# Kernel optimization log

Hardware: AMD Instinct MI355X
Metric: run time of the kernel (lower is better)

Reference implementation:

```python
import jax, jax.numpy as jnp
import numpy as np

NEG_FILL = jnp.finfo(jnp.float32).min  # stands in for tf.float64.min (overflows to -inf in f32)


def setup_inputs() -> dict:
    key = jax.random.key(0)
    k0, k1, k2, k3, k4 = jax.random.split(key, 5)
    B, N, E, D = 4, 4096, 1024, 256
    STD = 0.05  # tf.random_normal_initializer default stddev
    inputs = jax.random.normal(k0, (B, N, E), dtype=jnp.float32)
    Wq = STD * jax.random.normal(k1, (E, D), dtype=jnp.float32)
    Wk = STD * jax.random.normal(k2, (E, D), dtype=jnp.float32)
    Wvdown = STD * jax.random.normal(k3, (E, D), dtype=jnp.float32)
    Wvup = STD * jax.random.normal(k4, (D, E), dtype=jnp.float32)
    return {"inputs": inputs, "Wq": Wq, "Wk": Wk, "Wvdown": Wvdown, "Wvup": Wvup}


def reference(inputs, Wq, Wk, Wvdown, Wvup):
    B, N, E = inputs.shape
    D = Wq.shape[1]
    Q = inputs @ Wq                                   # [B, N, D]
    K = inputs @ Wk                                   # [B, N, D]
    score = jnp.einsum("bqd,bkd->bqk", Q, K)          # [B, N, N]
    score = score / jnp.sqrt(jnp.float32(D))
    # tf.linalg.band_part(score, -1, 0): keep lower triangle (causal)
    causal = jnp.tril(jnp.ones((N, N), dtype=bool))
    score = jnp.where(causal, score, 0.0)
    # original quirk: any exactly-zero entry (including masked ones) -> huge negative
    score = jnp.where(score != 0, score, NEG_FILL)
    attn = jax.nn.softmax(score, axis=-1)             # [B, N, N]
    V = inputs @ (Wvdown @ Wvup)                      # low-rank value proj, [B, N, E]
    return attn @ V                                   # [B, N, E]
```

## Files before the change

kernel.cpp:

```cpp
#include <hip/hip_runtime.h>
#include <hip/hip_bf16.h>


typedef __hip_bfloat16 bf16;
typedef __bf16 bf16x4 __attribute__((ext_vector_type(4)));
typedef __bf16 bf16x8 __attribute__((ext_vector_type(8)));
typedef float f32x4 __attribute__((ext_vector_type(4)));

#define BK 32
#define HALF_BYTES 8192
#define PVBUF 49152

__device__ __forceinline__ void gload_lds16(const bf16* g, bf16* l) {
    __builtin_amdgcn_global_load_lds(
        (const __attribute__((address_space(1))) unsigned int*)g,
        (__attribute__((address_space(3))) unsigned int*)l, 16, 0, 0);
}

__device__ __forceinline__ void zero_acc(f32x4 acc[4][4]) {
#pragma unroll
    for (int mi = 0; mi < 4; ++mi)
#pragma unroll
        for (int ni = 0; ni < 4; ++ni) {
            f32x4 zf = {0.f, 0.f, 0.f, 0.f};
            acc[mi][ni] = zf;
        }
}

__device__ __forceinline__ void mm_tile(const bf16* __restrict__ Ablk,
                                        const bf16* __restrict__ Bblk,
                                        int lda, int ldb, int kiters,
                                        bf16* As, bf16* Bs, f32x4 acc[4][4]) {
    const int tid  = threadIdx.x;
    const int wave = tid >> 6;
    const int lane = tid & 63;

    const int F0 = wave * 2048 + lane * 16;
    const int F1 = F0 + 1024;
    const int r0 = F0 >> 6, c0 = (F0 & 63) >> 1;
    const int r1 = F1 >> 6, c1 = (F1 & 63) >> 1;
    const bf16* ga0 = Ablk + (size_t)r0 * lda + c0;
    const bf16* ga1 = Ablk + (size_t)r1 * lda + c1;
    const bf16* gb0 = Bblk + (size_t)r0 * ldb + c0;
    const bf16* gb1 = Bblk + (size_t)r1 * ldb + c1;

    const int waveM = wave >> 1, waveN = wave & 1;
    const int mrow = waveM * 64 + (lane & 15);
    const int nrow = waveN * 64 + (lane & 15);
    const int koff = (lane >> 4) * 8;

#define STAGE_TO(buf)                                                        \
    {                                                                        \
        char* Ad = (char*)As + (buf) * HALF_BYTES;                           \
        char* Bd = (char*)Bs + (buf) * HALF_BYTES;                           \
        gload_lds16(ga0, (bf16*)(Ad + F0));                                  \
        gload_lds16(ga1, (bf16*)(Ad + F1));                                  \
        gload_lds16(gb0, (bf16*)(Bd + F0));                                  \
        gload_lds16(gb1, (bf16*)(Bd + F1));                                  \
        ga0 += BK; ga1 += BK; gb0 += BK; gb1 += BK;                          \
    }

    STAGE_TO(0);
    int cur = 0;
    for (int it = 0; it < kiters - 1; ++it) {
        const int nxt = cur ^ 1;
        STAGE_TO(nxt);

        __builtin_amdgcn_sched_barrier(0);
        asm volatile("s_waitcnt vmcnt(4)" ::: "memory");
        __builtin_amdgcn_sched_barrier(0);
        __builtin_amdgcn_s_barrier();
        __builtin_amdgcn_sched_barrier(0);

        {
            const bf16* Ar = (const bf16*)((const char*)As + cur * HALF_BYTES);
            const bf16* Br = (const bf16*)((const char*)Bs + cur * HALF_BYTES);
            bf16x8 af[4], bfr[4];
#pragma unroll
            for (int mi = 0; mi < 4; ++mi)
                af[mi] = *(const bf16x8*)(Ar + (mrow + mi * 16) * BK + koff);
#pragma unroll
            for (int ni = 0; ni < 4; ++ni)
                bfr[ni] = *(const bf16x8*)(Br + (nrow + ni * 16) * BK + koff);
#pragma unroll
            for (int mi = 0; mi < 4; ++mi)
#pragma unroll
                for (int ni = 0; ni < 4; ++ni)
                    acc[mi][ni] = __builtin_amdgcn_mfma_f32_16x16x32_bf16(
                        af[mi], bfr[ni], acc[mi][ni], 0, 0, 0);
        }

        __builtin_amdgcn_sched_barrier(0);
        asm volatile("s_waitcnt lgkmcnt(0)" ::: "memory");
        __builtin_amdgcn_sched_barrier(0);
        __builtin_amdgcn_s_barrier();
        __builtin_amdgcn_sched_barrier(0);
        cur = nxt;
    }

    __builtin_amdgcn_sched_barrier(0);
    asm volatile("s_waitcnt vmcnt(0)" ::: "memory");
    __builtin_amdgcn_sched_barrier(0);
    __builtin_amdgcn_s_barrier();
    __builtin_amdgcn_sched_barrier(0);
    {
        const bf16* Ar = (const bf16*)((const char*)As + cur * HALF_BYTES);
        const bf16* Br = (const bf16*)((const char*)Bs + cur * HALF_BYTES);
        bf16x8 af[4], bfr[4];
#pragma unroll
        for (int mi = 0; mi < 4; ++mi)
            af[mi] = *(const bf16x8*)(Ar + (mrow + mi * 16) * BK + koff);
#pragma unroll
        for (int ni = 0; ni < 4; ++ni)
            bfr[ni] = *(const bf16x8*)(Br + (nrow + ni * 16) * BK + koff);
#pragma unroll
        for (int mi = 0; mi < 4; ++mi)
#pragma unroll
            for (int ni = 0; ni < 4; ++ni)
                acc[mi][ni] = __builtin_amdgcn_mfma_f32_16x16x32_bf16(
                    af[mi], bfr[ni], acc[mi][ni], 0, 0, 0);
    }
#undef STAGE_TO
}

__global__ __launch_bounds__(256, 2) void k_gemm_plain(
    const bf16* __restrict__ A, long long aBatch,
    const bf16* __restrict__ BT, long long bBatch,
    bf16* __restrict__ C, long long cBatch,
    int lda, int ldb, int ldc, int kiters) {
    __shared__ __align__(16) bf16 As[2 * 128 * BK];
    __shared__ __align__(16) bf16 Bs[2 * 128 * BK];
    const int nBase = blockIdx.x * 128;
    const int mBase = blockIdx.y * 128;
    const int z = blockIdx.z;
    const bf16* Ab = A + (size_t)z * aBatch + (size_t)mBase * lda;
    const bf16* Bb = BT + (size_t)z * bBatch + (size_t)nBase * ldb;

    f32x4 acc[4][4];
    zero_acc(acc);
    mm_tile(Ab, Bb, lda, ldb, kiters, As, Bs, acc);

    const int tid = threadIdx.x, wave = tid >> 6, lane = tid & 63;
    const int waveM = wave >> 1, waveN = wave & 1;
    const int quad = lane >> 4, cno = lane & 15;
    bf16* Cb = C + (size_t)z * cBatch;
#pragma unroll
    for (int mi = 0; mi < 4; ++mi) {
        int row0 = mBase + waveM * 64 + mi * 16 + quad * 4;
#pragma unroll
        for (int ni = 0; ni < 4; ++ni) {
            int col = nBase + waveN * 64 + ni * 16 + cno;
#pragma unroll
            for (int r = 0; r < 4; ++r)
                Cb[(size_t)(row0 + r) * ldc + col] = __float2bfloat16(acc[mi][ni][r]);
        }
    }
}

#define P_BATCH 8650752ll
__global__ __launch_bounds__(256, 2) void k_score(
    const bf16* __restrict__ Qm, const bf16* __restrict__ Km,
    bf16* __restrict__ P, float* __restrict__ lsum) {
    const int f = blockIdx.x, b = blockIdx.z;
    int qt = (int)((sqrtf(8.f * (float)f + 1.f) - 1.f) * 0.5f);
    while ((qt + 1) * (qt + 2) / 2 <= f) ++qt;
    while (qt * (qt + 1) / 2 > f) --qt;
    const int kt = f - qt * (qt + 1) / 2;

    __shared__ __align__(16) bf16 As[2 * 128 * BK];
    __shared__ __align__(16) bf16 Bs[2 * 128 * BK];

    const bf16* Ab = Qm + ((size_t)b * 4096 + (size_t)qt * 128) * 256;
    const bf16* Bb = Km + ((size_t)b * 4096 + (size_t)kt * 128) * 256;

    f32x4 acc[4][4];
    zero_acc(acc);
    mm_tile(Ab, Bb, 256, 256, 256 / BK, As, Bs, acc);

    const int tid = threadIdx.x, wave = tid >> 6, lane = tid & 63;
    const int waveM = wave >> 1, waveN = wave & 1;
    const int quad = lane >> 4, cno = lane & 15;
    const int pitch = (qt + 1) * 128;
    bf16* Pb = P + b * P_BATCH + (size_t)16384 * (qt * (qt + 1) / 2);
    float* lb = lsum + b * 4096;
#pragma unroll
    for (int mi = 0; mi < 4; ++mi) {
        const int lq0 = waveM * 64 + mi * 16 + quad * 4;
        float rs[4] = {0.f, 0.f, 0.f, 0.f};
#pragma unroll
        for (int ni = 0; ni < 4; ++ni) {
            const int cn = waveN * 64 + ni * 16 + cno;
            const int gk = kt * 128 + cn;
#pragma unroll
            for (int r = 0; r < 4; ++r) {
                const int gq = qt * 128 + lq0 + r;
                float s = acc[mi][ni][r] * 0.0625f;
                float p = (gk <= gq && s != 0.0f) ? __expf(s) : 0.0f;
                bf16 pb = __float2bfloat16(p);
                Pb[(size_t)(lq0 + r) * pitch + gk] = pb;
                rs[r] += __bfloat162float(pb);
            }
        }
#pragma unroll
        for (int r = 0; r < 4; ++r) {
            float v = rs[r];
            v += __shfl_xor(v, 1);
            v += __shfl_xor(v, 2);
            v += __shfl_xor(v, 4);
            v += __shfl_xor(v, 8);
            if (cno == 0) atomicAdd(&lb[qt * 128 + lq0 + r], v);
        }
    }
}

__global__ __launch_bounds__(512, 2) void k_pv(
    const bf16* __restrict__ Pm, const bf16* __restrict__ VT,
    const float* __restrict__ lsum, float* __restrict__ Out) {
    __shared__ __align__(16) char lds[3 * PVBUF];
    const int l = blockIdx.x;
    const int p = l & 7, dv = (l >> 3) & 7, b = l >> 6;
    const int tid = threadIdx.x;
    const int wave = tid >> 6, lane = tid & 63;
    const int waveM = wave >> 1, waveN = wave & 1;
    const int quad = lane >> 4, cno = lane & 15;

    const int srow = tid >> 3;
    const int swzEl = (((tid & 7) * 16) ^ ((srow & 7) << 4)) >> 1;
    const int F = tid * 16;

    const bf16* VTb = VT + ((size_t)b * 1024 + dv * 128) * 4096;
    float* Ob = Out + (size_t)b * 4096 * 1024;
    const float* lb = lsum + b * 4096;

    const int rswz = (lane & 7) << 4;
    int offA[4], offB[4], colk[2];
#pragma unroll
    for (int mi = 0; mi < 4; ++mi)
        offA[mi] = (waveM * 64 + mi * 16 + (lane & 15)) * 128;
#pragma unroll
    for (int ni = 0; ni < 4; ++ni)
        offB[ni] = (waveN * 64 + ni * 16 + (lane & 15)) * 128;
    colk[0] = (quad * 16) ^ rswz;
    colk[1] = (64 + quad * 16) ^ rswz;

    const int Qv0 = p, Qv1 = 15 - p;
#pragma unroll 1
    for (int c = 0; c < 2; ++c) {
        const int Q = c ? Qv1 : Qv0;
        const int qt0 = 2 * Q;
        const int pitch1 = (qt0 + 1) * 128;
        const int pitch2 = (qt0 + 2) * 128;
        const bf16* base1 = Pm + (size_t)b * P_BATCH
                            + (size_t)16384 * (qt0 * (qt0 + 1) / 2);
        const bf16* base2 = Pm + (size_t)b * P_BATCH
                            + (size_t)16384 * ((qt0 + 1) * (qt0 + 2) / 2);
        const int nt = (qt0 + 2) * 2;

        const bf16* a0 = base1 + (size_t)srow * pitch1 + swzEl;
        const bf16* a1 = base1 + (size_t)(64 + srow) * pitch1 + swzEl;
        const bf16* a2 = base2 + (size_t)srow * pitch2 + swzEl;
        const bf16* a3 = base2 + (size_t)(64 + srow) * pitch2 + swzEl;
        const bf16* b0 = VTb + (size_t)srow * 4096 + swzEl;
        const bf16* b1 = VTb + (size_t)(64 + srow) * 4096 + swzEl;

        __builtin_amdgcn_s_barrier();

#define STG(bi)                                                              \
    {                                                                        \
        char* Ad = lds + (bi) * PVBUF;                                       \
        char* Bd = Ad + 32768;                                               \
        gload_lds16(a0, (bf16*)(Ad + F));                                    \
        gload_lds16(a1, (bf16*)(Ad + 8192 + F));                             \
        gload_lds16(a2, (bf16*)(Ad + 16384 + F));                            \
        gload_lds16(a3, (bf16*)(Ad + 24576 + F));                            \
        gload_lds16(b0, (bf16*)(Bd + F));                                    \
        gload_lds16(b1, (bf16*)(Bd + 8192 + F));                             \
        a0 += 64; a1 += 64; a2 += 64; a3 += 64; b0 += 64; b1 += 64;          \
    }

        f32x4 acc[4][4];
        zero_acc(acc);
        STG(0);
        STG(1);
        int buf = 0;
        for (int t = 0; t < nt; ++t) {
            __builtin_amdgcn_sched_barrier(0);
            if (t < nt - 1)
                asm volatile("s_waitcnt vmcnt(6)" ::: "memory");
            else
                asm volatile("s_waitcnt vmcnt(0)" ::: "memory");
            __builtin_amdgcn_sched_barrier(0);
            __builtin_amdgcn_s_barrier();
            __builtin_amdgcn_sched_barrier(0);
            if (t + 2 < nt) {
                int bi = buf + 2; if (bi >= 3) bi -= 3;
                STG(bi);
            }
            if (!(waveM < 2 && t >= nt - 2)) {
                const char* Ab = lds + buf * PVBUF;
                const char* Bd = Ab + 32768;
#pragma unroll
                for (int kk = 0; kk < 2; ++kk) {
                    bf16x8 af[4], bfv[4];
#pragma unroll
                    for (int mi = 0; mi < 4; ++mi)
                        af[mi] = *(const bf16x8*)(Ab + offA[mi] + colk[kk]);
#pragma unroll
                    for (int ni = 0; ni < 4; ++ni)
                        bfv[ni] = *(const bf16x8*)(Bd + offB[ni] + colk[kk]);
                    __builtin_amdgcn_s_setprio(1);
#pragma unroll
                    for (int mi = 0; mi < 4; ++mi)
#pragma unroll
                        for (int ni = 0; ni < 4; ++ni)
                            acc[mi][ni] =
                                __builtin_amdgcn_mfma_f32_16x16x32_bf16(
                                    af[mi], bfv[ni], acc[mi][ni], 0, 0, 0);
                    __builtin_amdgcn_s_setprio(0);
                }
            }
            buf = (buf + 1 == 3) ? 0 : buf + 1;
        }
#undef STG

#pragma unroll
        for (int mi = 0; mi < 4; ++mi) {
            const int lq0 = waveM * 64 + mi * 16 + quad * 4;
#pragma unroll
            for (int r = 0; r < 4; ++r) {
                const int gq = Q * 256 + lq0 + r;
                const float inv = 1.0f / lb[gq];
#pragma unroll
                for (int ni = 0; ni < 4; ++ni) {
                    const int col = dv * 128 + waveN * 64 + ni * 16 + cno;
                    Ob[(size_t)gq * 1024 + col] = acc[mi][ni][r] * inv;
                }
            }
        }
    }
}

__global__ void k_cast(const float4* __restrict__ in, bf16* __restrict__ out,
                       int n4) {
    int i = blockIdx.x * 256 + threadIdx.x;
    if (i >= n4) return;
    float4 v = in[i];
    bf16x4 o;
    o[0] = (__bf16)v.x; o[1] = (__bf16)v.y; o[2] = (__bf16)v.z; o[3] = (__bf16)v.w;
    *(bf16x4*)(out + 4 * (size_t)i) = o;
}

__global__ void k_transpose(const float* __restrict__ in, bf16* __restrict__ out,
                            int n, int mask, int shift, int tstride) {
    int idx = blockIdx.x * 256 + threadIdx.x;
    if (idx >= n) return;
    out[idx] = __float2bfloat16(in[(size_t)(idx & mask) * tstride + (idx >> shift)]);
}

extern "C" void kernel_launch(void* const* d_in, const int* in_sizes, int n_in,
                              void* d_out, int out_size, void* d_ws, size_t ws_size,
                              hipStream_t stream) {
    const int B = 4, N = 4096, E = 1024, D = 256;
    const float* X   = (const float*)d_in[0];
    const float* Wq  = (const float*)d_in[1];
    const float* Wk  = (const float*)d_in[2];
    const float* Wvd = (const float*)d_in[3];
    const float* Wvu = (const float*)d_in[4];
    float* out = (float*)d_out;

    const long long MiB = 1ll << 20;
    char* ws = (char*)d_ws;
    bf16* Xb     = (bf16*)(ws);
    bf16* WqT    = (bf16*)(ws + 32 * MiB);
    bf16* WkT    = (bf16*)(ws + 32 * MiB + 524288);
    bf16* WvdT   = (bf16*)(ws + 32 * MiB + 1048576);
    bf16* WvupT  = (bf16*)(ws + 32 * MiB + 1572864);
    bf16* P      = (bf16*)(ws);
    bf16* Qm     = (bf16*)(ws + 66 * MiB);
    bf16* Km     = (bf16*)(ws + 74 * MiB);
    bf16* Vd     = (bf16*)(ws + 82 * MiB);
    bf16* VT     = (bf16*)(ws + 90 * MiB);
    float* lsum  = (float*)(ws + 122 * MiB);

    const int n4 = B * N * E / 4;
    k_cast<<<(n4 + 255) / 256, 256, 0, stream>>>((const float4*)X, Xb, n4);
    k_transpose<<<1024, 256, 0, stream>>>(Wq,  WqT,  E * D, 1023, 10, 256);
    k_transpose<<<1024, 256, 0, stream>>>(Wk,  WkT,  E * D, 1023, 10, 256);
    k_transpose<<<1024, 256, 0, stream>>>(Wvd, WvdT, E * D, 1023, 10, 256);
    k_transpose<<<1024, 256, 0, stream>>>(Wvu, WvupT, D * E, 255, 8, 1024);
    hipMemsetAsync(lsum, 0, (size_t)B * N * sizeof(float), stream);

    k_gemm_plain<<<dim3(D / 128, (B * N) / 128, 3), 256, 0, stream>>>(
        Xb, 0, WqT, (long long)D * E, Qm, (long long)B * N * D,
        E, E, D, E / BK);

    k_gemm_plain<<<dim3(N / 128, E / 128, B), 256, 0, stream>>>(
        WvupT, 0, Vd, (long long)N * D, VT, (long long)E * N,
        D, D, N, D / BK);

    k_score<<<dim3(528, 1, B), 256, 0, stream>>>(Qm, Km, P, lsum);

    k_pv<<<dim3(256, 1, 1), 512, 0, stream>>>(P, VT, lsum, out);
}
```

Measured before the change: 313.5 us.

## Shrink PV kernel to 128x128 tiles with double-buffered loads and more blocks

The P·V kernel moves from 512-thread blocks computing a 256-row query tile (two stacked 128-row P panels) with a triple-buffered LDS pipeline to 256-thread blocks computing a 128x128 output tile with a double-buffered pipeline. Each block pairs query tile qt with 31-qt for causal load balance, and the grid grows from 256 to 512 blocks. The aim is finer-grained work distribution and lower LDS use per block. The trade-off is an extra barrier per K-step, less prefetch depth, and V tiles now reused by only 128 rows instead of 256.

```diff
diff --git a/kernel.cpp b/kernel.cpp
--- a/kernel.cpp
+++ b/kernel.cpp
@@ -9,7 +9,7 @@
 
 #define BK 32
 #define HALF_BYTES 8192
-#define PVBUF 49152
+#define PVBUF 32768
 
 __device__ __forceinline__ void gload_lds16(const bf16* g, bf16* l) {
     __builtin_amdgcn_global_load_lds(
@@ -213,12 +213,12 @@
     }
 }
 
-__global__ __launch_bounds__(512, 2) void k_pv(
+__global__ __launch_bounds__(256, 2) void k_pv(
     const bf16* __restrict__ Pm, const bf16* __restrict__ VT,
     const float* __restrict__ lsum, float* __restrict__ Out) {
-    __shared__ __align__(16) char lds[3 * PVBUF];
+    __shared__ __align__(16) char lds[2 * PVBUF];
     const int l = blockIdx.x;
-    const int p = l & 7, dv = (l >> 3) & 7, b = l >> 6;
+    const int pr = l & 15, dv = (l >> 4) & 7, b = l >> 7;
     const int tid = threadIdx.x;
     const int wave = tid >> 6, lane = tid & 63;
     const int waveM = wave >> 1, waveN = wave & 1;
@@ -243,92 +243,99 @@
     colk[0] = (quad * 16) ^ rswz;
     colk[1] = (64 + quad * 16) ^ rswz;
 
-    const int Qv0 = p, Qv1 = 15 - p;
 #pragma unroll 1
     for (int c = 0; c < 2; ++c) {
-        const int Q = c ? Qv1 : Qv0;
-        const int qt0 = 2 * Q;
-        const int pitch1 = (qt0 + 1) * 128;
-        const int pitch2 = (qt0 + 2) * 128;
-        const bf16* base1 = Pm + (size_t)b * P_BATCH
-                            + (size_t)16384 * (qt0 * (qt0 + 1) / 2);
-        const bf16* base2 = Pm + (size_t)b * P_BATCH
-                            + (size_t)16384 * ((qt0 + 1) * (qt0 + 2) / 2);
-        const int nt = (qt0 + 2) * 2;
-
-        const bf16* a0 = base1 + (size_t)srow * pitch1 + swzEl;
-        const bf16* a1 = base1 + (size_t)(64 + srow) * pitch1 + swzEl;
-        const bf16* a2 = base2 + (size_t)srow * pitch2 + swzEl;
-        const bf16* a3 = base2 + (size_t)(64 + srow) * pitch2 + swzEl;
+        const int qt = c ? (31 - pr) : pr;
+        const int pitch = (qt + 1) * 128;
+        const bf16* base = Pm + (size_t)b * P_BATCH
+                           + (size_t)16384 * (qt * (qt + 1) / 2);
+        const int nt = (qt + 1) * 2;
+
+        const bf16* a0 = base + (size_t)srow * pitch + swzEl;
+        const bf16* a1 = base + (size_t)(32 + srow) * pitch + swzEl;
+        const bf16* a2 = base + (size_t)(64 + srow) * pitch + swzEl;
+        const bf16* a3 = base + (size_t)(96 + srow) * pitch + swzEl;
         const bf16* b0 = VTb + (size_t)srow * 4096 + swzEl;
-        const bf16* b1 = VTb + (size_t)(64 + srow) * 4096 + swzEl;
+        const bf16* b1 = VTb + (size_t)(32 + srow) * 4096 + swzEl;
+        const bf16* b2 = VTb + (size_t)(64 + srow) * 4096 + swzEl;
+        const bf16* b3 = VTb + (size_t)(96 + srow) * 4096 + swzEl;
 
         __builtin_amdgcn_s_barrier();
 
 #define STG(bi)                                                              \
     {                                                                        \
         char* Ad = lds + (bi) * PVBUF;                                       \
-        char* Bd = Ad + 32768;                                               \
+        char* Bd = Ad + 16384;                                               \
         gload_lds16(a0, (bf16*)(Ad + F));                                    \
-        gload_lds16(a1, (bf16*)(Ad + 8192 + F));                             \
-        gload_lds16(a2, (bf16*)(Ad + 16384 + F));                            \
-        gload_lds16(a3, (bf16*)(Ad + 24576 + F));                            \
+        gload_lds16(a1, (bf16*)(Ad + 4096 + F));                             \
+        gload_lds16(a2, (bf16*)(Ad + 8192 + F));                             \
+        gload_lds16(a3, (bf16*)(Ad + 12288 + F));                            \
         gload_lds16(b0, (bf16*)(Bd + F));                                    \
-        gload_lds16(b1, (bf16*)(Bd + 8192 + F));                             \
-        a0 += 64; a1 += 64; a2 += 64; a3 += 64; b0 += 64; b1 += 64;          \
+        gload_lds16(b1, (bf16*)(Bd + 4096 + F));                             \
+        gload_lds16(b2, (bf16*)(Bd + 8192 + F));                             \
+        gload_lds16(b3, (bf16*)(Bd + 12288 + F));                            \
+        a0 += 64; a1 += 64; a2 += 64; a3 += 64;                              \
+        b0 += 64; b1 += 64; b2 += 64; b3 += 64;                              \
+    }
+
+#define COMPUTE(bi)                                                          \
+    {                                                                        \
+        const char* Ab = lds + (bi) * PVBUF;                                 \
+        const char* Bd = Ab + 16384;                                         \
+        _Pragma("unroll")                                                    \
+        for (int kk = 0; kk < 2; ++kk) {                                     \
+            bf16x8 af[4], bfv[4];                                            \
+            _Pragma("unroll")                                                \
+            for (int mi = 0; mi < 4; ++mi)                                   \
+                af[mi] = *(const bf16x8*)(Ab + offA[mi] + colk[kk]);         \
+            _Pragma("unroll")                                                \
+            for (int ni = 0; ni < 4; ++ni)                                   \
+                bfv[ni] = *(const bf16x8*)(Bd + offB[ni] + colk[kk]);        \
+            __builtin_amdgcn_s_setprio(1);                                   \
+            _Pragma("unroll")                                                \
+            for (int mi = 0; mi < 4; ++mi)                                   \
+                _Pragma("unroll")                                            \
+                for (int ni = 0; ni < 4; ++ni)                               \
+                    acc[mi][ni] = __builtin_amdgcn_mfma_f32_16x16x32_bf16(   \
+                        af[mi], bfv[ni], acc[mi][ni], 0, 0, 0);              \
+            __builtin_amdgcn_s_setprio(0);                                   \
+        }                                                                    \
     }
 
         f32x4 acc[4][4];
         zero_acc(acc);
         STG(0);
-        STG(1);
-        int buf = 0;
-        for (int t = 0; t < nt; ++t) {
-            __builtin_amdgcn_sched_barrier(0);
-            if (t < nt - 1)
-                asm volatile("s_waitcnt vmcnt(6)" ::: "memory");
-            else
-                asm volatile("s_waitcnt vmcnt(0)" ::: "memory");
+        int cur = 0;
+        for (int t = 0; t < nt - 1; ++t) {
+            STG(cur ^ 1);
+            __builtin_amdgcn_sched_barrier(0);
+            asm volatile("s_waitcnt vmcnt(8)" ::: "memory");
             __builtin_amdgcn_sched_barrier(0);
             __builtin_amdgcn_s_barrier();
             __builtin_amdgcn_sched_barrier(0);
-            if (t + 2 < nt) {
-                int bi = buf + 2; if (bi >= 3) bi -= 3;
-                STG(bi);
-            }
-            if (!(waveM < 2 && t >= nt - 2)) {
-                const char* Ab = lds + buf * PVBUF;
-                const char* Bd = Ab + 32768;
-#pragma unroll
-                for (int kk = 0; kk < 2; ++kk) {
-                    bf16x8 af[4], bfv[4];
-#pragma unroll
-                    for (int mi = 0; mi < 4; ++mi)
-                        af[mi] = *(const bf16x8*)(Ab + offA[mi] + colk[kk]);
-#pragma unroll
-                    for (int ni = 0; ni < 4; ++ni)
-                        bfv[ni] = *(const bf16x8*)(Bd + offB[ni] + colk[kk]);
-                    __builtin_amdgcn_s_setprio(1);
-#pragma unroll
-                    for (int mi = 0; mi < 4; ++mi)
-#pragma unroll
-                        for (int ni = 0; ni < 4; ++ni)
-                            acc[mi][ni] =
-                                __builtin_amdgcn_mfma_f32_16x16x32_bf16(
-                                    af[mi], bfv[ni], acc[mi][ni], 0, 0, 0);
-                    __builtin_amdgcn_s_setprio(0);
-                }
-            }
-            buf = (buf + 1 == 3) ? 0 : buf + 1;
-        }
+            COMPUTE(cur);
+            __builtin_amdgcn_sched_barrier(0);
+            asm volatile("s_waitcnt lgkmcnt(0)" ::: "memory");
+            __builtin_amdgcn_sched_barrier(0);
+            __builtin_amdgcn_s_barrier();
+            __builtin_amdgcn_sched_barrier(0);
+            cur ^= 1;
+        }
+        __builtin_amdgcn_sched_barrier(0);
+        asm volatile("s_waitcnt vmcnt(0)" ::: "memory");
+        __builtin_amdgcn_sched_barrier(0);
+        __builtin_amdgcn_s_barrier();
+        __builtin_amdgcn_sched_barrier(0);
+        COMPUTE(cur);
 #undef STG
+#undef COMPUTE
 
 #pragma unroll
         for (int mi = 0; mi < 4; ++mi) {
             const int lq0 = waveM * 64 + mi * 16 + quad * 4;
 #pragma unroll
             for (int r = 0; r < 4; ++r) {
-                const int gq = Q * 256 + lq0 + r;
+                const int gq = qt * 128 + lq0 + r;
                 const float inv = 1.0f / lb[gq];
 #pragma unroll
                 for (int ni = 0; ni < 4; ++ni) {
@@ -400,5 +407,5 @@
 
     k_score<<<dim3(528, 1, B), 256, 0, stream>>>(Qm, Km, P, lsum);
 
-    k_pv<<<dim3(256, 1, 1), 512, 0, stream>>>(P, VT, lsum, out);
-}
+    k_pv<<<dim3(512, 1, 1), 256, 0, stream>>>(P, VT, lsum, out);
+}
```

Result: slower. 329.2 us (+5.0%).
